# Kernel tuning notes

Measured on AMD Instinct MI355X. Metric: run time of the kernel, lower is better.

Reference implementation:

```python
import jax, jax.numpy as jnp
import numpy as np

N, C_IN, C_OUT, T, V = 256, 64, 64, 64, 25
REL = C_IN // 8  # rel_channels = in_channels // rel_reduction (in_channels != 3)


def setup_inputs() -> dict:
    key = jax.random.key(0)
    ks = jax.random.split(key, 10)
    s_in = 1.0 / np.sqrt(C_IN)
    s_rel = 1.0 / np.sqrt(REL)
    return {
        "x": jax.random.normal(ks[0], (N, C_IN, T, V), dtype=jnp.float32),
        "A": jax.random.normal(ks[1], (V, V), dtype=jnp.float32),
        "w1": jax.random.normal(ks[2], (REL, C_IN), dtype=jnp.float32) * s_in,
        "b1": jnp.zeros((REL,), dtype=jnp.float32),
        "w2": jax.random.normal(ks[3], (REL, C_IN), dtype=jnp.float32) * s_in,
        "b2": jnp.zeros((REL,), dtype=jnp.float32),
        "w3": jax.random.normal(ks[4], (C_OUT, REL), dtype=jnp.float32) * s_rel,
        "b3": jnp.zeros((C_OUT,), dtype=jnp.float32),
        "wr": jax.random.normal(ks[5], (C_OUT, C_IN), dtype=jnp.float32) * s_in,
        "br": jnp.zeros((C_OUT,), dtype=jnp.float32),
    }


def reference(x, A, w1, b1, w2, b2, w3, b3, wr, br):
    alpha = 1.0
    # residual: 1x1 conv over channels -> (N, C_OUT, T, V)
    inputs = jnp.einsum('oi,nitv->notv', wr, x) + br[None, :, None, None]
    # conv1/conv2 then temporal mean -> (N, REL, V)
    x1 = jnp.einsum('ri,nitv->nrv', w1, x) / T + b1[None, :, None]
    x2 = jnp.einsum('ri,nitv->nrv', w2, x) / T + b2[None, :, None]
    # broadcast outer difference -> (N, REL, V, V)
    d = jnp.tanh(x1[:, :, :, None] - x2[:, :, None, :])
    # conv3 (1x1 over rel channels) -> (N, C_OUT, V, V); add static A
    Adyn = jnp.einsum('or,nruv->nouv', w3, d) + b3[None, :, None, None]
    Afull = Adyn * alpha + A[None, None, :, :]
    # per-channel batched graph conv: (N,C,V,V) x (N,C,T,V) -> (N,C,T,V)
    out = jnp.einsum('ncuv,nctv->nctu', Afull, inputs)
    return out
```

## Files before the change

kernel.cpp:

```cpp
#include <hip/hip_runtime.h>
#include <cmath>

namespace {
constexpr int NB  = 256;
constexpr int CI  = 64;
constexpr int CO  = 64;
constexpr int TT  = 64;
constexpr int V   = 25;
constexpr int REL = 8;
constexpr int TV  = TT * V;
constexpr int CC  = 8;
constexpr int IP  = 28;
constexpr int AP  = 28;
}

typedef float f4 __attribute__((ext_vector_type(4)));

__global__ __launch_bounds__(1024) void k1_x12(
    const float* __restrict__ x,
    const float* __restrict__ w1, const float* __restrict__ b1,
    const float* __restrict__ w2, const float* __restrict__ b2,
    float* __restrict__ ws) {
  const int n = blockIdx.x;
  const int tid = threadIdx.x;
  __shared__ __align__(16) float xs[8][TV];
  __shared__ float xsum[CI][V];
  __shared__ float w12[2][REL][CI];

  for (int idx = tid; idx < 2 * REL * CI; idx += 1024) {
    int half = idx / (REL * CI), rem = idx % (REL * CI);
    w12[half][rem / CI][rem % CI] = half ? w2[rem] : w1[rem];
  }

  const float4* xb = reinterpret_cast<const float4*>(x + (size_t)n * (CI * TV));
  float4* xsv = reinterpret_cast<float4*>(&xs[0][0]);
  constexpr int V4G = 8 * TV / 4;

  for (int g = 0; g < 8; ++g) {
    __syncthreads();
    for (int idx = tid; idx < V4G; idx += 1024)
      xsv[idx] = xb[g * V4G + idx];
    __syncthreads();
    if (tid < 8 * V) {
      int ch = tid / V, v = tid % V;
      float acc = 0.f;
      #pragma unroll
      for (int t = 0; t < TT; ++t) acc += xs[ch][t * V + v];
      xsum[g * 8 + ch][v] = acc;
    }
  }
  __syncthreads();

  if (tid < 2 * REL * V) {
    int half = tid / (REL * V), rem = tid % (REL * V);
    int r = rem / V, v = rem % V;
    float a = 0.f;
    #pragma unroll
    for (int i = 0; i < CI; ++i) a = fmaf(w12[half][r][i], xsum[i][v], a);
    ws[(size_t)n * (2 * REL * V) + tid] = a * (1.f / TT) + (half ? b2[r] : b1[r]);
  }
}

__global__ __launch_bounds__(512, 4) void k2_fused(
    const float* __restrict__ x, const float* __restrict__ A,
    const float* __restrict__ w3, const float* __restrict__ b3,
    const float* __restrict__ wr, const float* __restrict__ br,
    const float* __restrict__ ws, float* __restrict__ out) {
  const int id  = blockIdx.x;
  const int n   = (id & 7) | ((id >> 3) & ~7);
  const int cb  = (id >> 3) & 7;
  const int c0  = cb * CC;
  const int tid = threadIdx.x;

  __shared__ __align__(16) float inp[CC * TT * IP];
  __shared__ __align__(16) float Afs[CC * V * AP];

  {
    f4* iz = reinterpret_cast<f4*>(inp);
    #pragma unroll
    for (int k = 0; k < CC * TT * IP / 4 / 512; ++k)
      iz[tid + k * 512] = (f4)0.f;
  }

  const float* x1n = ws + (size_t)n * (2 * REL * V);
  const float* x2n = x1n + REL * V;
  for (int idx = tid; idx < V * AP; idx += 512) {
    int u = idx / AP, v = idx % AP;
    if (v < V) {
      float t8[REL];
      #pragma unroll
      for (int r = 0; r < REL; ++r)
        t8[r] = tanhf(x1n[r * V + u] - x2n[r * V + v]);
      const float base = A[u * V + v];
      #pragma unroll
      for (int cc = 0; cc < CC; ++cc) {
        float acc = base + b3[c0 + cc];
        #pragma unroll
        for (int r = 0; r < REL; ++r)
          acc = fmaf(w3[(c0 + cc) * REL + r], t8[r], acc);
        Afs[(cc * V + u) * AP + v] = acc;
      }
    } else {
      #pragma unroll
      for (int cc = 0; cc < CC; ++cc)
        Afs[(cc * V + u) * AP + v] = 0.f;
    }
  }
  __syncthreads();

  if (tid < TV / 4) {
    const float* xp = x + (size_t)n * (CI * TV) + tid * 4;
    float acc[CC][4];
    #pragma unroll
    for (int cc = 0; cc < CC; ++cc) {
      float b = br[c0 + cc];
      acc[cc][0] = b; acc[cc][1] = b; acc[cc][2] = b; acc[cc][3] = b;
    }
    #pragma unroll 4
    for (int i = 0; i < CI; ++i) {
      float4 xv = *reinterpret_cast<const float4*>(xp + (size_t)i * TV);
      float w8[CC];
      #pragma unroll
      for (int cc = 0; cc < CC; ++cc)
        w8[cc] = wr[(size_t)(c0 + cc) * CI + i];
      #pragma unroll
      for (int cc = 0; cc < CC; ++cc) {
        acc[cc][0] = fmaf(w8[cc], xv.x, acc[cc][0]);
        acc[cc][1] = fmaf(w8[cc], xv.y, acc[cc][1]);
        acc[cc][2] = fmaf(w8[cc], xv.z, acc[cc][2]);
        acc[cc][3] = fmaf(w8[cc], xv.w, acc[cc][3]);
      }
    }
    int tv0 = tid * 4;
    int t = tv0 / V, v = tv0 % V;
    #pragma unroll
    for (int k = 0; k < 4; ++k) {
      #pragma unroll
      for (int cc = 0; cc < CC; ++cc)
        inp[(cc * TT + t) * IP + v] = acc[cc][k];
      if (++v == V) { v = 0; ++t; }
    }
  }
  __syncthreads();

  const int cc = tid >> 6;
  const int tq = (tid >> 2) & 15;
  const int uq = tid & 3;
  const int u0 = uq * 6;

  float acc[4][7];
  #pragma unroll
  for (int a = 0; a < 4; ++a)
    #pragma unroll
    for (int b = 0; b < 7; ++b) acc[a][b] = 0.f;

  const float* ib = &inp[(cc * TT + tq) * IP];
  const float* ab = &Afs[(cc * V + u0) * AP];

  #pragma unroll
  for (int chk = 0; chk < 7; ++chk) {
    const f4 x0 = *reinterpret_cast<const f4*>(ib + 0 * 16 * IP + chk * 4);
    const f4 x1 = *reinterpret_cast<const f4*>(ib + 1 * 16 * IP + chk * 4);
    const f4 x2 = *reinterpret_cast<const f4*>(ib + 2 * 16 * IP + chk * 4);
    const f4 x3 = *reinterpret_cast<const f4*>(ib + 3 * 16 * IP + chk * 4);
    #pragma unroll
    for (int ku = 0; ku < 7; ++ku) {
      const f4 a = *reinterpret_cast<const f4*>(ab + ku * AP + chk * 4);
      acc[0][ku] = fmaf(a.w, x0.w, fmaf(a.z, x0.z, fmaf(a.y, x0.y, fmaf(a.x, x0.x, acc[0][ku]))));
      acc[1][ku] = fmaf(a.w, x1.w, fmaf(a.z, x1.z, fmaf(a.y, x1.y, fmaf(a.x, x1.x, acc[1][ku]))));
      acc[2][ku] = fmaf(a.w, x2.w, fmaf(a.z, x2.z, fmaf(a.y, x2.y, fmaf(a.x, x2.x, acc[2][ku]))));
      acc[3][ku] = fmaf(a.w, x3.w, fmaf(a.z, x3.z, fmaf(a.y, x3.y, fmaf(a.x, x3.x, acc[3][ku]))));
    }
  }

  float* ob = out + ((size_t)n * CO + (c0 + cc)) * (TT * V);
  #pragma unroll
  for (int ti = 0; ti < 4; ++ti) {
    const int t = tq + 16 * ti;
    #pragma unroll
    for (int ku = 0; ku < 7; ++ku)
      ob[t * V + u0 + ku] = acc[ti][ku];
  }
}

extern "C" void kernel_launch(void* const* d_in, const int* in_sizes, int n_in,
                              void* d_out, int out_size, void* d_ws, size_t ws_size,
                              hipStream_t stream) {
  (void)in_sizes; (void)n_in; (void)out_size; (void)ws_size;
  const float* x  = (const float*)d_in[0];
  const float* A  = (const float*)d_in[1];
  const float* w1 = (const float*)d_in[2];
  const float* b1 = (const float*)d_in[3];
  const float* w2 = (const float*)d_in[4];
  const float* b2 = (const float*)d_in[5];
  const float* w3 = (const float*)d_in[6];
  const float* b3 = (const float*)d_in[7];
  const float* wr = (const float*)d_in[8];
  const float* br = (const float*)d_in[9];
  float* out = (float*)d_out;
  float* ws  = (float*)d_ws;

  hipLaunchKernelGGL(k1_x12, dim3(NB), dim3(1024), 0, stream,
                     x, w1, b1, w2, b2, ws);
  hipLaunchKernelGGL(k2_fused, dim3(NB * CO / CC), dim3(512), 0, stream,
                     x, A, w3, b3, wr, br, ws, out);
}
```

Baseline: 145.6 us.

## Use fast tanh, zero only pad columns, deepen unroll, remap graph-conv thread tiling

Replaces tanhf with an exp-based fast tanh and zeroes only the three padding columns of each shared input row instead of clearing the whole buffer. It raises the unroll factor of the residual channel loop and changes the graph-conv stage so that 256 threads each compute 8x7 outputs instead of 512 threads each computing 4x7. The intent is to cut transcendental cost, shared-memory stores and redundant A-tile loads. The trade-off is that half the threads sit idle in the final stage and register pressure rises, which may hurt latency hiding.

```diff
diff --git a/kernel.cpp b/kernel.cpp
--- a/kernel.cpp
+++ b/kernel.cpp
@@ -16,6 +16,13 @@
 
 typedef float f4 __attribute__((ext_vector_type(4)));
 
+__device__ __forceinline__ float fast_tanh(float x) {
+  float ax = fabsf(x);
+  float e  = __expf(-2.f * ax);
+  float r  = (1.f - e) / (1.f + e);
+  return copysignf(r, x);
+}
+
 __global__ __launch_bounds__(1024) void k1_x12(
     const float* __restrict__ x,
     const float* __restrict__ w1, const float* __restrict__ b1,
@@ -76,10 +83,8 @@
   __shared__ __align__(16) float Afs[CC * V * AP];
 
   {
-    f4* iz = reinterpret_cast<f4*>(inp);
-    #pragma unroll
-    for (int k = 0; k < CC * TT * IP / 4 / 512; ++k)
-      iz[tid + k * 512] = (f4)0.f;
+    float* row = inp + tid * IP;
+    row[25] = 0.f; row[26] = 0.f; row[27] = 0.f;
   }
 
   const float* x1n = ws + (size_t)n * (2 * REL * V);
@@ -90,7 +95,7 @@
       float t8[REL];
       #pragma unroll
       for (int r = 0; r < REL; ++r)
-        t8[r] = tanhf(x1n[r * V + u] - x2n[r * V + v]);
+        t8[r] = fast_tanh(x1n[r * V + u] - x2n[r * V + v]);
       const float base = A[u * V + v];
       #pragma unroll
       for (int cc = 0; cc < CC; ++cc) {
@@ -116,7 +121,7 @@
       float b = br[c0 + cc];
       acc[cc][0] = b; acc[cc][1] = b; acc[cc][2] = b; acc[cc][3] = b;
     }
-    #pragma unroll 4
+    #pragma unroll 8
     for (int i = 0; i < CI; ++i) {
       float4 xv = *reinterpret_cast<const float4*>(xp + (size_t)i * TV);
       float w8[CC];
@@ -143,43 +148,47 @@
   }
   __syncthreads();
 
-  const int cc = tid >> 6;
-  const int tq = (tid >> 2) & 15;
-  const int uq = tid & 3;
-  const int u0 = uq * 6;
-
-  float acc[4][7];
-  #pragma unroll
-  for (int a = 0; a < 4; ++a)
-    #pragma unroll
-    for (int b = 0; b < 7; ++b) acc[a][b] = 0.f;
-
-  const float* ib = &inp[(cc * TT + tq) * IP];
-  const float* ab = &Afs[(cc * V + u0) * AP];
-
-  #pragma unroll
-  for (int chk = 0; chk < 7; ++chk) {
-    const f4 x0 = *reinterpret_cast<const f4*>(ib + 0 * 16 * IP + chk * 4);
-    const f4 x1 = *reinterpret_cast<const f4*>(ib + 1 * 16 * IP + chk * 4);
-    const f4 x2 = *reinterpret_cast<const f4*>(ib + 2 * 16 * IP + chk * 4);
-    const f4 x3 = *reinterpret_cast<const f4*>(ib + 3 * 16 * IP + chk * 4);
-    #pragma unroll
-    for (int ku = 0; ku < 7; ++ku) {
-      const f4 a = *reinterpret_cast<const f4*>(ab + ku * AP + chk * 4);
-      acc[0][ku] = fmaf(a.w, x0.w, fmaf(a.z, x0.z, fmaf(a.y, x0.y, fmaf(a.x, x0.x, acc[0][ku]))));
-      acc[1][ku] = fmaf(a.w, x1.w, fmaf(a.z, x1.z, fmaf(a.y, x1.y, fmaf(a.x, x1.x, acc[1][ku]))));
-      acc[2][ku] = fmaf(a.w, x2.w, fmaf(a.z, x2.z, fmaf(a.y, x2.y, fmaf(a.x, x2.x, acc[2][ku]))));
-      acc[3][ku] = fmaf(a.w, x3.w, fmaf(a.z, x3.z, fmaf(a.y, x3.y, fmaf(a.x, x3.x, acc[3][ku]))));
-    }
-  }
-
-  float* ob = out + ((size_t)n * CO + (c0 + cc)) * (TT * V);
-  #pragma unroll
-  for (int ti = 0; ti < 4; ++ti) {
-    const int t = tq + 16 * ti;
-    #pragma unroll
-    for (int ku = 0; ku < 7; ++ku)
-      ob[t * V + u0 + ku] = acc[ti][ku];
+  if (tid < 256) {
+    const int cc = tid >> 5;
+    const int tq = (tid >> 2) & 7;
+    const int uq = tid & 3;
+    const int u0 = uq * 6;
+
+    float acc[8][7];
+    #pragma unroll
+    for (int a = 0; a < 8; ++a)
+      #pragma unroll
+      for (int b = 0; b < 7; ++b) acc[a][b] = 0.f;
+
+    const float* ib = &inp[(cc * TT + tq) * IP];
+    const float* ab = &Afs[(cc * V + u0) * AP];
+
+    #pragma unroll
+    for (int chk = 0; chk < 7; ++chk) {
+      f4 xr[8];
+      #pragma unroll
+      for (int ti = 0; ti < 8; ++ti)
+        xr[ti] = *reinterpret_cast<const f4*>(ib + ti * 8 * IP + chk * 4);
+      #pragma unroll
+      for (int ku = 0; ku < 7; ++ku) {
+        const f4 a = *reinterpret_cast<const f4*>(ab + ku * AP + chk * 4);
+        #pragma unroll
+        for (int ti = 0; ti < 8; ++ti)
+          acc[ti][ku] = fmaf(a.w, xr[ti].w,
+                        fmaf(a.z, xr[ti].z,
+                        fmaf(a.y, xr[ti].y,
+                        fmaf(a.x, xr[ti].x, acc[ti][ku]))));
+      }
+    }
+
+    float* ob = out + ((size_t)n * CO + (c0 + cc)) * (size_t)(TT * V);
+    #pragma unroll
+    for (int ti = 0; ti < 8; ++ti) {
+      const int t = tq + 8 * ti;
+      #pragma unroll
+      for (int ku = 0; ku < 7; ++ku)
+        ob[t * V + u0 + ku] = acc[ti][ku];
+    }
   }
 }
 
```

Measured after the change: 176.9 us. 21.5% more time.
